# Performance work log

Hardware: AMD Instinct MI355X
Metric: run time of the kernel (lower is better)

Reference implementation:

```python
import jax, jax.numpy as jnp
import numpy as np

N_NODES = 50000
N_EDGES = 800000
D = 128  # d_feat == hidden_channels


def setup_inputs() -> dict:
    key = jax.random.key(0)
    ks = jax.random.split(key, 7)
    s = 1.0 / np.sqrt(D)
    return {
        "x": jax.random.normal(ks[0], (N_NODES, D), dtype=jnp.float32),
        "edge_index": jax.random.randint(ks[1], (2, N_EDGES), 0, N_NODES, dtype=jnp.int64),
        "W1_l": jax.random.normal(ks[2], (D, D), dtype=jnp.float32) * s,
        "b1": jnp.zeros((D,), dtype=jnp.float32),
        "W1_r": jax.random.normal(ks[3], (D, D), dtype=jnp.float32) * s,
        "W2_l": jax.random.normal(ks[4], (D, D), dtype=jnp.float32) * s,
        "b2": jnp.zeros((D,), dtype=jnp.float32),
        "W2_r": jax.random.normal(ks[5], (D, D), dtype=jnp.float32) * s,
    }


def reference(x, edge_index, W1_l, b1, W1_r, W2_l, b2, W2_r):
    src = edge_index[0]
    dst = edge_index[1]
    n = x.shape[0]
    # in-degree for mean aggregation (zero-degree nodes get 0 aggregate)
    deg = jax.ops.segment_sum(jnp.ones_like(src, dtype=x.dtype), dst, num_segments=n)
    inv_deg = (1.0 / jnp.maximum(deg, 1.0))[:, None]  # [N,1]

    def sage_conv(h, Wl, b, Wr):
        # mean over incoming neighbor messages, then lin_l(agg) + lin_r(h)
        agg = jax.ops.segment_sum(h[src], dst, num_segments=n) * inv_deg  # [N,D]
        return agg @ Wl + b + h @ Wr

    h = jax.nn.relu(sage_conv(x, W1_l, b1, W1_r))
    return sage_conv(h, W2_l, b2, W2_r)
```

## Files before the change

kernel.cpp:

```cpp
#include <hip/hip_runtime.h>
#include <hip/hip_bf16.h>

typedef __attribute__((ext_vector_type(8))) short bf16x8;
typedef __attribute__((ext_vector_type(4))) float f32x4;

#define CAP 64
#define SH  8

static __device__ inline unsigned short f2b(float f) {
    unsigned u = __float_as_uint(f);
    unsigned r = (u + 0x7FFFu + ((u >> 16) & 1u)) >> 16;
    return (unsigned short)r;
}
static __device__ inline float blo(unsigned u) { return __uint_as_float(u << 16); }
static __device__ inline float bhi(unsigned u) { return __uint_as_float(u & 0xFFFF0000u); }

__global__ void zero_kernel(int* __restrict__ p, int n) {
    int i = blockIdx.x * blockDim.x + threadIdx.x;
    if (i < n) p[i] = 0;
}

__global__ __launch_bounds__(256) void fill_shard_kernel(
        const int* __restrict__ ei, int* __restrict__ cursor,
        unsigned short* __restrict__ edge16, int E, int N, int G, int npg) {
    int s = blockIdx.x & (SH - 1);
    int i = blockIdx.x >> 3;
    int d_lo = s * npg;
    int d_hi = d_lo + npg; if (d_hi > N) d_hi = N;
    int C = (E + G - 1) / G;
    int e0 = i * C;
    int e1 = e0 + C; if (e1 > E) e1 = E;
    for (int e = e0 + threadIdx.x; e < e1; e += 256) {
        int d = ei[E + e];
        if (d < d_lo || d >= d_hi) continue;
        int src = ei[e];
        if ((unsigned)src >= (unsigned)N) src = 0;
        int pos = atomicAdd(&cursor[d], 1);
        if (pos < CAP) edge16[(size_t)d * CAP + pos] = (unsigned short)src;
    }
}

__global__ __launch_bounds__(256) void x2b_kernel(const float* __restrict__ x,
                                                  unsigned short* __restrict__ xb,
                                                  int n4) {
    int i = blockIdx.x * blockDim.x + threadIdx.x;
    if (i >= n4) return;
    float4 v = ((const float4*)x)[i];
    ushort4 b;
    b.x = f2b(v.x); b.y = f2b(v.y); b.z = f2b(v.z); b.w = f2b(v.w);
    ((ushort4*)xb)[i] = b;
}

__global__ __launch_bounds__(256) void aggregate_kernel(
        const unsigned short* __restrict__ in, const int* __restrict__ cursor,
        const unsigned short* __restrict__ edge16, const int* __restrict__ ei,
        unsigned short* __restrict__ agg, int E, int N) {
    int node = blockIdx.x * 4 + (threadIdx.x >> 6);
    if (node >= N) return;
    int lane = threadIdx.x & 63;
    int g = lane >> 4;
    int f = lane & 15;
    int deg = cursor[node];

    float acc[8];
    #pragma unroll
    for (int i = 0; i < 8; ++i) acc[i] = 0.f;

    if (deg <= CAP) {
        const unsigned short* base = edge16 + (size_t)node * CAP;
        int idx = (lane < deg) ? (int)base[lane] : 0;
        #pragma unroll 4
        for (int j = 0; j < deg; j += 4) {
            int e = j + g;
            int s = __shfl(idx, e & 63);
            if (e < deg) {
                uint4 v = *(const uint4*)(in + (size_t)s * 128 + f * 8);
                acc[0] += blo(v.x); acc[1] += bhi(v.x);
                acc[2] += blo(v.y); acc[3] += bhi(v.y);
                acc[4] += blo(v.z); acc[5] += bhi(v.z);
                acc[6] += blo(v.w); acc[7] += bhi(v.w);
            }
        }
    } else {
        for (int j = 0; j < E; j += 4) {
            int e = j + g;
            bool act = (e < E) && (ei[E + e] == node);
            if (act) {
                int s = ei[e];
                if ((unsigned)s >= (unsigned)N) s = 0;
                uint4 v = *(const uint4*)(in + (size_t)s * 128 + f * 8);
                acc[0] += blo(v.x); acc[1] += bhi(v.x);
                acc[2] += blo(v.y); acc[3] += bhi(v.y);
                acc[4] += blo(v.z); acc[5] += bhi(v.z);
                acc[6] += blo(v.w); acc[7] += bhi(v.w);
            }
        }
    }

    #pragma unroll
    for (int d = 16; d <= 32; d <<= 1) {
        #pragma unroll
        for (int i = 0; i < 8; ++i) acc[i] += __shfl_xor(acc[i], d);
    }

    if (g == 0) {
        float inv = 1.0f / (float)(deg > 1 ? deg : 1);
        uint4 o;
        o.x = (unsigned)f2b(acc[0] * inv) | ((unsigned)f2b(acc[1] * inv) << 16);
        o.y = (unsigned)f2b(acc[2] * inv) | ((unsigned)f2b(acc[3] * inv) << 16);
        o.z = (unsigned)f2b(acc[4] * inv) | ((unsigned)f2b(acc[5] * inv) << 16);
        o.w = (unsigned)f2b(acc[6] * inv) | ((unsigned)f2b(acc[7] * inv) << 16);
        *(uint4*)(agg + (size_t)node * 128 + f * 8) = o;
    }
}

__global__ void prep_w_kernel(const float* __restrict__ W1l, const float* __restrict__ W1r,
                              const float* __restrict__ W2l, const float* __restrict__ W2r,
                              unsigned short* __restrict__ wt) {
    int n = blockIdx.x & 127;
    int layer = blockIdx.x >> 7;
    int k = threadIdx.x;
    const float* Wlp = layer ? W2l : W1l;
    const float* Wrp = layer ? W2r : W1r;
    unsigned short* dst = wt + (size_t)layer * 128 * 256 + (size_t)n * 256;
    dst[k]       = f2b(Wlp[(size_t)k * 128 + n]);
    dst[k + 128] = f2b(Wrp[(size_t)k * 128 + n]);
}

template<int RELU, int OUT_BF16>
__global__ __launch_bounds__(256) void gemm_mfma_kernel(
        const unsigned short* __restrict__ Arow, const unsigned short* __restrict__ Xrow,
        const unsigned short* __restrict__ Wt, const float* __restrict__ bias,
        void* __restrict__ outp, int n) {
    constexpr int LDK = 264;
    __shared__ unsigned short sA[64 * LDK];
    int tid = threadIdx.x;
    int row0 = blockIdx.x * 64;

    #pragma unroll
    for (int it = 0; it < 8; ++it) {
        int c = tid + it * 256;
        int r = c >> 5;
        int q = c & 31;
        int row = row0 + r; if (row >= n) row = n - 1;
        uint4 v = (q < 16) ? ((const uint4*)(Arow + (size_t)row * 128))[q]
                           : ((const uint4*)(Xrow + (size_t)row * 128))[q - 16];
        *(uint4*)&sA[r * LDK + q * 8] = v;
    }
    __syncthreads();

    int lane = tid & 63;
    int wave = tid >> 6;
    int quad = lane >> 4;
    int tm   = lane & 15;

    f32x4 acc[4][2];
    #pragma unroll
    for (int m = 0; m < 4; ++m)
        #pragma unroll
        for (int j = 0; j < 2; ++j)
            acc[m][j] = (f32x4){0.f, 0.f, 0.f, 0.f};

    const unsigned short* wb0 = Wt + (size_t)(wave * 32 + tm) * 256;

    #pragma unroll
    for (int ks = 0; ks < 8; ++ks) {
        int k0 = ks * 32 + quad * 8;
        bf16x8 a[4], b[2];
        #pragma unroll
        for (int m = 0; m < 4; ++m)
            a[m] = *(const bf16x8*)&sA[(m * 16 + tm) * LDK + k0];
        #pragma unroll
        for (int j = 0; j < 2; ++j)
            b[j] = *(const bf16x8*)(wb0 + (size_t)j * 16 * 256 + k0);
        #pragma unroll
        for (int m = 0; m < 4; ++m)
            #pragma unroll
            for (int j = 0; j < 2; ++j)
                acc[m][j] = __builtin_amdgcn_mfma_f32_16x16x32_bf16(a[m], b[j], acc[m][j], 0, 0, 0);
    }

    #pragma unroll
    for (int j = 0; j < 2; ++j) {
        int ncol = wave * 32 + j * 16 + tm;
        float bb = bias[ncol];
        #pragma unroll
        for (int m = 0; m < 4; ++m) {
            #pragma unroll
            for (int reg = 0; reg < 4; ++reg) {
                int row = row0 + m * 16 + quad * 4 + reg;
                if (row >= n) continue;
                float v = acc[m][j][reg] + bb;
                if (RELU) v = v > 0.f ? v : 0.f;
                if (OUT_BF16)
                    ((unsigned short*)outp)[(size_t)row * 128 + ncol] = f2b(v);
                else
                    ((float*)outp)[(size_t)row * 128 + ncol] = v;
            }
        }
    }
}

extern "C" void kernel_launch(void* const* d_in, const int* in_sizes, int n_in,
                              void* d_out, int out_size, void* d_ws, size_t ws_size,
                              hipStream_t stream) {
    const float* x   = (const float*)d_in[0];
    const int*   ei  = (const int*)d_in[1];
    const float* W1l = (const float*)d_in[2];
    const float* b1  = (const float*)d_in[3];
    const float* W1r = (const float*)d_in[4];
    const float* W2l = (const float*)d_in[5];
    const float* b2  = (const float*)d_in[6];
    const float* W2r = (const float*)d_in[7];
    float* out = (float*)d_out;

    const int D = 128;
    const int N = in_sizes[0] / D;
    const int E = in_sizes[1] / 2;

    char* ws = (char*)d_ws;
    size_t off = 0;
    auto alloc = [&](size_t bytes) {
        size_t o = off;
        off = (off + bytes + 511) & ~(size_t)511;
        return (void*)(ws + o);
    };
    int*            cursor  = (int*)           alloc((size_t)N * 4);
    unsigned short* edge16  = (unsigned short*)alloc((size_t)N * CAP * 2);
    unsigned short* agg_bf  = (unsigned short*)alloc((size_t)N * D * 2);
    unsigned short* xb      = (unsigned short*)alloc((size_t)N * D * 2);
    unsigned short* wt      = (unsigned short*)alloc((size_t)2 * 128 * 256 * 2);
    unsigned short* h_bf = xb;
    (void)ws_size; (void)n_in; (void)out_size;

    zero_kernel<<<(N + 255) / 256, 256, 0, stream>>>(cursor, N);
    {
        int G = 256;
        int npg = (N + SH - 1) / SH;
        fill_shard_kernel<<<SH * G, 256, 0, stream>>>(ei, cursor, edge16, E, N, G, npg);
    }

    int n4 = N * D / 4;
    x2b_kernel<<<(n4 + 255) / 256, 256, 0, stream>>>(x, xb, n4);
    prep_w_kernel<<<256, 128, 0, stream>>>(W1l, W1r, W2l, W2r, wt);
    const unsigned short* wt1 = wt;
    const unsigned short* wt2 = wt + (size_t)128 * 256;

    int agg_grid  = (N + 3) / 4;
    int gemm_grid = (N + 63) / 64;

    aggregate_kernel<<<agg_grid, 256, 0, stream>>>(xb, cursor, edge16, ei, agg_bf, E, N);
    gemm_mfma_kernel<1, 1><<<gemm_grid, 256, 0, stream>>>(agg_bf, xb, wt1, b1, (void*)h_bf, N);

    aggregate_kernel<<<agg_grid, 256, 0, stream>>>(h_bf, cursor, edge16, ei, agg_bf, E, N);
    gemm_mfma_kernel<0, 0><<<gemm_grid, 256, 0, stream>>>(agg_bf, h_bf, wt2, b2, (void*)out, N);
}
```

Baseline: 230.3 us.

## Split aggregation feature dimension into four column slices across blocks

The aggregate kernel now launches four times as many blocks, each handling a 32-column slice of the 128-wide bf16 feature row. Each wave processes 8 edges at a time with 8-byte loads per lane instead of 4 edges with 16-byte loads. The aim is more parallelism and, since slice-major block ordering means concurrent blocks touch one 64-byte slice of all rows, better cache locality per pass. The cost is that the edge list and degree are read four times and each gather moves smaller chunks.

```diff
diff --git a/kernel.cpp b/kernel.cpp
--- a/kernel.cpp
+++ b/kernel.cpp
@@ -6,6 +6,7 @@
 
 #define CAP 64
 #define SH  8
+#define SLICES 4
 
 static __device__ inline unsigned short f2b(float f) {
     unsigned u = __float_as_uint(f);
@@ -54,63 +55,58 @@
 __global__ __launch_bounds__(256) void aggregate_kernel(
         const unsigned short* __restrict__ in, const int* __restrict__ cursor,
         const unsigned short* __restrict__ edge16, const int* __restrict__ ei,
-        unsigned short* __restrict__ agg, int E, int N) {
-    int node = blockIdx.x * 4 + (threadIdx.x >> 6);
+        unsigned short* __restrict__ agg, int E, int N, int nb4) {
+    int slice = blockIdx.x / nb4;
+    int blk   = blockIdx.x - slice * nb4;
+    int node  = blk * 4 + (threadIdx.x >> 6);
     if (node >= N) return;
     int lane = threadIdx.x & 63;
-    int g = lane >> 4;
-    int f = lane & 15;
+    int g = lane >> 3;
+    int f = lane & 7;
     int deg = cursor[node];
 
-    float acc[8];
-    #pragma unroll
-    for (int i = 0; i < 8; ++i) acc[i] = 0.f;
+    float acc[4] = {0.f, 0.f, 0.f, 0.f};
+    const unsigned short* inS = in + slice * 32;
 
     if (deg <= CAP) {
         const unsigned short* base = edge16 + (size_t)node * CAP;
         int idx = (lane < deg) ? (int)base[lane] : 0;
-        #pragma unroll 4
-        for (int j = 0; j < deg; j += 4) {
+        #pragma unroll 2
+        for (int j = 0; j < deg; j += 8) {
             int e = j + g;
             int s = __shfl(idx, e & 63);
             if (e < deg) {
-                uint4 v = *(const uint4*)(in + (size_t)s * 128 + f * 8);
+                uint2 v = *(const uint2*)(inS + (size_t)s * 128 + f * 4);
                 acc[0] += blo(v.x); acc[1] += bhi(v.x);
                 acc[2] += blo(v.y); acc[3] += bhi(v.y);
-                acc[4] += blo(v.z); acc[5] += bhi(v.z);
-                acc[6] += blo(v.w); acc[7] += bhi(v.w);
             }
         }
     } else {
-        for (int j = 0; j < E; j += 4) {
+        for (int j = 0; j < E; j += 8) {
             int e = j + g;
             bool act = (e < E) && (ei[E + e] == node);
             if (act) {
                 int s = ei[e];
                 if ((unsigned)s >= (unsigned)N) s = 0;
-                uint4 v = *(const uint4*)(in + (size_t)s * 128 + f * 8);
+                uint2 v = *(const uint2*)(inS + (size_t)s * 128 + f * 4);
                 acc[0] += blo(v.x); acc[1] += bhi(v.x);
                 acc[2] += blo(v.y); acc[3] += bhi(v.y);
-                acc[4] += blo(v.z); acc[5] += bhi(v.z);
-                acc[6] += blo(v.w); acc[7] += bhi(v.w);
             }
         }
     }
 
     #pragma unroll
-    for (int d = 16; d <= 32; d <<= 1) {
-        #pragma unroll
-        for (int i = 0; i < 8; ++i) acc[i] += __shfl_xor(acc[i], d);
+    for (int d = 8; d <= 32; d <<= 1) {
+        #pragma unroll
+        for (int i = 0; i < 4; ++i) acc[i] += __shfl_xor(acc[i], d);
     }
 
     if (g == 0) {
         float inv = 1.0f / (float)(deg > 1 ? deg : 1);
-        uint4 o;
+        uint2 o;
         o.x = (unsigned)f2b(acc[0] * inv) | ((unsigned)f2b(acc[1] * inv) << 16);
         o.y = (unsigned)f2b(acc[2] * inv) | ((unsigned)f2b(acc[3] * inv) << 16);
-        o.z = (unsigned)f2b(acc[4] * inv) | ((unsigned)f2b(acc[5] * inv) << 16);
-        o.w = (unsigned)f2b(acc[6] * inv) | ((unsigned)f2b(acc[7] * inv) << 16);
-        *(uint4*)(agg + (size_t)node * 128 + f * 8) = o;
+        *(uint2*)(agg + (size_t)node * 128 + slice * 32 + f * 4) = o;
     }
 }
 
@@ -246,12 +242,13 @@
     const unsigned short* wt1 = wt;
     const unsigned short* wt2 = wt + (size_t)128 * 256;
 
-    int agg_grid  = (N + 3) / 4;
+    int nb4       = (N + 3) / 4;
+    int agg_grid  = SLICES * nb4;
     int gemm_grid = (N + 63) / 64;
 
-    aggregate_kernel<<<agg_grid, 256, 0, stream>>>(xb, cursor, edge16, ei, agg_bf, E, N);
+    aggregate_kernel<<<agg_grid, 256, 0, stream>>>(xb, cursor, edge16, ei, agg_bf, E, N, nb4);
     gemm_mfma_kernel<1, 1><<<gemm_grid, 256, 0, stream>>>(agg_bf, xb, wt1, b1, (void*)h_bf, N);
 
-    aggregate_kernel<<<agg_grid, 256, 0, stream>>>(h_bf, cursor, edge16, ei, agg_bf, E, N);
+    aggregate_kernel<<<agg_grid, 256, 0, stream>>>(h_bf, cursor, edge16, ei, agg_bf, E, N, nb4);
     gemm_mfma_kernel<0, 0><<<gemm_grid, 256, 0, stream>>>(agg_bf, h_bf, wt2, b2, (void*)out, N);
 }
```

Measured after the change: 306.5 us. 33.1% more time.

## Map one 16-lane group per node in aggregation, removing cross-group reduction

Applied to the files above, without the earlier changes.

The aggregation kernel now assigns each 16-lane quarter-wave its own destination node instead of splitting one node's edges across four groups. This drops the shuffle-xor reduction and the idle lanes at the store, and uses packed f32x2 accumulation. The trade-offs are serial per-node edge loops, so lanes sharing a wave diverge when degrees differ, and a slower overflow path that scans every edge per node. Each block now covers 16 nodes.

```diff
diff --git a/kernel.cpp b/kernel.cpp
--- a/kernel.cpp
+++ b/kernel.cpp
@@ -3,6 +3,7 @@
 
 typedef __attribute__((ext_vector_type(8))) short bf16x8;
 typedef __attribute__((ext_vector_type(4))) float f32x4;
+typedef __attribute__((ext_vector_type(2))) float f32x2;
 
 #define CAP 64
 #define SH  8
@@ -55,63 +56,57 @@
         const unsigned short* __restrict__ in, const int* __restrict__ cursor,
         const unsigned short* __restrict__ edge16, const int* __restrict__ ei,
         unsigned short* __restrict__ agg, int E, int N) {
-    int node = blockIdx.x * 4 + (threadIdx.x >> 6);
+    int tid  = threadIdx.x;
+    int wave = tid >> 6;
+    int lane = tid & 63;
+    int g    = lane >> 4;
+    int fl   = lane & 15;
+    int node = blockIdx.x * 16 + wave * 4 + g;
     if (node >= N) return;
-    int lane = threadIdx.x & 63;
-    int g = lane >> 4;
-    int f = lane & 15;
     int deg = cursor[node];
 
-    float acc[8];
-    #pragma unroll
-    for (int i = 0; i < 8; ++i) acc[i] = 0.f;
+    f32x2 a01 = {0.f, 0.f}, a23 = {0.f, 0.f}, a45 = {0.f, 0.f}, a67 = {0.f, 0.f};
 
     if (deg <= CAP) {
         const unsigned short* base = edge16 + (size_t)node * CAP;
-        int idx = (lane < deg) ? (int)base[lane] : 0;
-        #pragma unroll 4
-        for (int j = 0; j < deg; j += 4) {
-            int e = j + g;
-            int s = __shfl(idx, e & 63);
-            if (e < deg) {
-                uint4 v = *(const uint4*)(in + (size_t)s * 128 + f * 8);
-                acc[0] += blo(v.x); acc[1] += bhi(v.x);
-                acc[2] += blo(v.y); acc[3] += bhi(v.y);
-                acc[4] += blo(v.z); acc[5] += bhi(v.z);
-                acc[6] += blo(v.w); acc[7] += bhi(v.w);
+        int idx[4];
+        #pragma unroll
+        for (int c = 0; c < 4; ++c) idx[c] = (int)base[c * 16 + fl];
+        #pragma unroll
+        for (int c = 0; c < 4; ++c) {
+            int j0 = c * 16;
+            if (deg <= j0) break;
+            int jend = deg < j0 + 16 ? deg : j0 + 16;
+            for (int j = j0; j < jend; ++j) {
+                int s = __shfl(idx[c], (g << 4) | (j - j0));
+                const uint4 v = *(const uint4*)(in + (size_t)s * 128 + fl * 8);
+                a01 += (f32x2){blo(v.x), bhi(v.x)};
+                a23 += (f32x2){blo(v.y), bhi(v.y)};
+                a45 += (f32x2){blo(v.z), bhi(v.z)};
+                a67 += (f32x2){blo(v.w), bhi(v.w)};
             }
         }
     } else {
-        for (int j = 0; j < E; j += 4) {
-            int e = j + g;
-            bool act = (e < E) && (ei[E + e] == node);
-            if (act) {
-                int s = ei[e];
+        for (int j = 0; j < E; ++j) {
+            if (ei[E + j] == node) {
+                int s = ei[j];
                 if ((unsigned)s >= (unsigned)N) s = 0;
-                uint4 v = *(const uint4*)(in + (size_t)s * 128 + f * 8);
-                acc[0] += blo(v.x); acc[1] += bhi(v.x);
-                acc[2] += blo(v.y); acc[3] += bhi(v.y);
-                acc[4] += blo(v.z); acc[5] += bhi(v.z);
-                acc[6] += blo(v.w); acc[7] += bhi(v.w);
+                const uint4 v = *(const uint4*)(in + (size_t)s * 128 + fl * 8);
+                a01 += (f32x2){blo(v.x), bhi(v.x)};
+                a23 += (f32x2){blo(v.y), bhi(v.y)};
+                a45 += (f32x2){blo(v.z), bhi(v.z)};
+                a67 += (f32x2){blo(v.w), bhi(v.w)};
             }
         }
     }
 
-    #pragma unroll
-    for (int d = 16; d <= 32; d <<= 1) {
-        #pragma unroll
-        for (int i = 0; i < 8; ++i) acc[i] += __shfl_xor(acc[i], d);
-    }
-
-    if (g == 0) {
-        float inv = 1.0f / (float)(deg > 1 ? deg : 1);
-        uint4 o;
-        o.x = (unsigned)f2b(acc[0] * inv) | ((unsigned)f2b(acc[1] * inv) << 16);
-        o.y = (unsigned)f2b(acc[2] * inv) | ((unsigned)f2b(acc[3] * inv) << 16);
-        o.z = (unsigned)f2b(acc[4] * inv) | ((unsigned)f2b(acc[5] * inv) << 16);
-        o.w = (unsigned)f2b(acc[6] * inv) | ((unsigned)f2b(acc[7] * inv) << 16);
-        *(uint4*)(agg + (size_t)node * 128 + f * 8) = o;
-    }
+    float inv = 1.0f / (float)(deg > 1 ? deg : 1);
+    uint4 o;
+    o.x = (unsigned)f2b(a01.x * inv) | ((unsigned)f2b(a01.y * inv) << 16);
+    o.y = (unsigned)f2b(a23.x * inv) | ((unsigned)f2b(a23.y * inv) << 16);
+    o.z = (unsigned)f2b(a45.x * inv) | ((unsigned)f2b(a45.y * inv) << 16);
+    o.w = (unsigned)f2b(a67.x * inv) | ((unsigned)f2b(a67.y * inv) << 16);
+    *(uint4*)(agg + (size_t)node * 128 + fl * 8) = o;
 }
 
 __global__ void prep_w_kernel(const float* __restrict__ W1l, const float* __restrict__ W1r,
@@ -246,7 +241,7 @@
     const unsigned short* wt1 = wt;
     const unsigned short* wt2 = wt + (size_t)128 * 256;
 
-    int agg_grid  = (N + 3) / 4;
+    int agg_grid  = (N + 15) / 16;
     int gemm_grid = (N + 63) / 64;
 
     aggregate_kernel<<<agg_grid, 256, 0, stream>>>(xb, cursor, edge16, ei, agg_bf, E, N);
```

Result: no change. 229.5 us (-0.3%).
